# Kernel optimization log

Measured on AMD Instinct MI355X. Metric: run time of the kernel, lower is better.

## Reference

```python
import jax, jax.numpy as jnp
import numpy as np

N, E = 50000, 800000
IN_C, EDGE_IN, HID, HEADS = 16, 16, 32, 4


def setup_inputs() -> dict:
    key = jax.random.key(0)
    ks = jax.random.split(key, 16)
    HC = HEADS * HID
    def lin(k, fan_in, shape):
        b = 1.0 / np.sqrt(fan_in)
        return jax.random.uniform(k, shape, jnp.float32, -b, b)
    return {
        "x": jax.random.normal(ks[0], (N, IN_C), jnp.float32),
        "edge_index": jax.random.randint(ks[1], (2, E), 0, N, jnp.int64),
        "edge_attr": jax.random.normal(ks[2], (E, EDGE_IN), jnp.float32),
        # TransformerConv params
        "Wq": lin(ks[3], IN_C, (IN_C, HC)), "bq": lin(ks[4], IN_C, (HC,)),
        "Wk": lin(ks[5], IN_C, (IN_C, HC)), "bk": lin(ks[6], IN_C, (HC,)),
        "Wv": lin(ks[7], IN_C, (IN_C, HC)), "bv": lin(ks[8], IN_C, (HC,)),
        "We": lin(ks[9], EDGE_IN, (EDGE_IN, HC)),  # lin_edge has no bias in PyG
        "Wskip": lin(ks[10], IN_C, (IN_C, HID)), "bskip": lin(ks[11], IN_C, (HID,)),
        # edge MLP params
        "W1": lin(ks[12], 2 * HID + EDGE_IN, (2 * HID + EDGE_IN, HID)),
        "b1": lin(ks[13], 2 * HID + EDGE_IN, (HID,)),
        "W2": lin(ks[14], HID, (HID, 1)), "b2": lin(ks[15], HID, (1,)),
    }


def _forward(x, edge_attr, Wq, bq, Wk, bk, Wv, bv, We, Wskip, bskip, W1, b1, W2, b2, src, dst):
    n = x.shape[0]
    q = (x @ Wq + bq).reshape(n, HEADS, HID)
    k = (x @ Wk + bk).reshape(n, HEADS, HID)
    v = (x @ Wv + bv).reshape(n, HEADS, HID)
    e = (edge_attr @ We).reshape(-1, HEADS, HID)  # [E,H,C]
    kj = k[src] + e                               # key of source node + edge emb
    alpha = jnp.einsum('ehc,ehc->eh', q[dst], kj) / jnp.sqrt(jnp.float32(HID))
    # segment softmax over incoming edges of each dst node (per head)
    m = jax.ops.segment_max(alpha, dst, num_segments=n)      # [N,H]
    a = jnp.exp(alpha - m[dst])
    s = jax.ops.segment_sum(a, dst, num_segments=n)          # [N,H]
    a = a / s[dst]
    msg = (v[src] + e) * a[:, :, None]                        # [E,H,C]
    out = jax.ops.segment_sum(msg, dst, num_segments=n)      # [N,H,C]
    out = out.mean(axis=1)                                    # concat=False -> mean over heads
    out = out + x @ Wskip + bskip                              # root/skip connection
    # edge MLP on gather-concat features
    feat = jnp.concatenate([out[src], edge_attr, out[dst]], axis=-1)
    h = jax.nn.relu(feat @ W1 + b1)
    return (h @ W2 + b2).reshape(-1)


def reference(x, edge_index, edge_attr, Wq, bq, Wk, bk, Wv, bv, We, Wskip, bskip, W1, b1, W2, b2):
    src, dst = edge_index[0], edge_index[1]
    return _forward(x, edge_attr, Wq, bq, Wk, bk, Wv, bv, We, Wskip, bskip, W1, b1, W2, b2, src, dst)
```

## Files before the change

### kernel.cpp

```cpp
#include <hip/hip_runtime.h>
#include <hip/hip_fp16.h>

#define NN 50000
#define NE 800000
#define NB 196
#define EPB 3125
#define NODE_BLOCKS 12500

#define SL 0.25506413f

#define PMV 0
#define MEV 1024
#define BEV 2048
#define UPV 2112
#define WPV 2176
#define WCV 2240
#define P_TOTAL 2304

template <int CTRL>
__device__ __forceinline__ float dpp_add(float v) {
  int m = __builtin_amdgcn_update_dpp(0, __builtin_bit_cast(int, v), CTRL, 0xF, 0xF, true);
  return v + __builtin_bit_cast(float, m);
}
__device__ __forceinline__ float row16_reduce(float v) {
  v = dpp_add<0xB1>(v);
  v = dpp_add<0x4E>(v);
  v = dpp_add<0x124>(v);
  v = dpp_add<0x128>(v);
  return v;
}

__global__ __launch_bounds__(256) void precompute_kernel(
    const float* __restrict__ Wq, const float* __restrict__ Wk,
    const float* __restrict__ bq, const float* __restrict__ bk,
    const float* __restrict__ We, float* __restrict__ P) {
  int t = threadIdx.x;
  for (int idx = t; idx < 1024; idx += 256) {
    int lane = idx >> 4, i = idx & 15;
    int h = lane >> 4, tt = lane & 15;
    float am = 0.f, ae = 0.f;
#pragma unroll
    for (int c = 0; c < 32; c++) {
      float wq = Wq[i * 128 + h * 32 + c];
      am += wq * Wk[tt * 128 + h * 32 + c];
      ae += wq * We[tt * 128 + h * 32 + c];
    }
    P[PMV + idx] = am * SL;
    P[MEV + idx] = ae * SL;
  }
  if (t < 64) {
    int h = t >> 4, tt = t & 15;
    float be = 0.f, up = 0.f, wp = 0.f;
#pragma unroll
    for (int c = 0; c < 32; c++) {
      be += bq[h * 32 + c] * We[tt * 128 + h * 32 + c];
      up += Wq[tt * 128 + h * 32 + c] * bk[h * 32 + c];
      wp += bq[h * 32 + c] * Wk[tt * 128 + h * 32 + c];
    }
    P[BEV + t] = be * SL;
    P[UPV + t] = up * SL;
    P[WPV + t] = wp * SL;
  }
  if (t < 4) {
    float wc = 0.f;
#pragma unroll
    for (int c = 0; c < 32; c++) wc += bq[t * 32 + c] * bk[t * 32 + c];
    P[WCV + t] = wc * SL;
  }
}

__global__ __launch_bounds__(256) void node_linear_kernel(
    const float* __restrict__ x, const float* __restrict__ P,
    const int* __restrict__ ei, int* __restrict__ hist_all,
    float* __restrict__ y, float* __restrict__ qe,
    float* __restrict__ u4, float* __restrict__ w4) {
  __shared__ int hist[NB];
  if (blockIdx.x >= NODE_BLOCKS) {
    int b = blockIdx.x - NODE_BLOCKS;
    int t = threadIdx.x;
    if (t < NB) hist[t] = 0;
    __syncthreads();
    int base = b * EPB;
    for (int i = t; i < EPB; i += 256)
      atomicAdd(&hist[ei[NE + base + i] >> 8], 1);
    __syncthreads();
    if (t < NB) hist_all[t * 256 + b] = hist[t];
    return;
  }
  int wave = threadIdx.x >> 6;
  int lane = threadIdx.x & 63;
  int n = blockIdx.x * 4 + wave;
  int h = lane >> 4, t = lane & 15;

  const float4* xp = (const float4*)(x + n * 16);
  float4 X0 = xp[0], X1 = xp[1], X2 = xp[2], X3 = xp[3];
  float xr[16] = {X0.x, X0.y, X0.z, X0.w, X1.x, X1.y, X1.z, X1.w,
                  X2.x, X2.y, X2.z, X2.w, X3.x, X3.y, X3.z, X3.w};

  const float4* pm = (const float4*)(P + PMV) + lane * 4;
  const float4* me = (const float4*)(P + MEV) + lane * 4;
  float yt = 0.f, qv = P[BEV + lane];
#pragma unroll
  for (int i4 = 0; i4 < 4; i4++) {
    float4 m = pm[i4], e = me[i4];
    yt += xr[4 * i4] * m.x + xr[4 * i4 + 1] * m.y
        + xr[4 * i4 + 2] * m.z + xr[4 * i4 + 3] * m.w;
    qv += xr[4 * i4] * e.x + xr[4 * i4 + 1] * e.y
        + xr[4 * i4 + 2] * e.z + xr[4 * i4 + 3] * e.w;
  }
  y[n * 64 + lane] = yt;
  qe[n * 64 + lane] = qv;

  float pu = P[UPV + lane] * xr[t];
  float pw = P[WPV + lane] * xr[t];
  pu = row16_reduce(pu);
  pw = row16_reduce(pw);
  if (t == 0) {
    u4[n * 4 + h] = pu;
    w4[n * 4 + h] = pw + P[WCV + h];
  }
}

__global__ __launch_bounds__(256) void scan_buckets_kernel(
    int* __restrict__ hist_all, int* __restrict__ btot) {
  int wv = blockIdx.x * 4 + (threadIdx.x >> 6);
  int l = threadIdx.x & 63;
  if (wv >= NB) return;
  int base = wv * 256;
  int run = 0;
#pragma unroll
  for (int c = 0; c < 4; c++) {
    int v = hist_all[base + c * 64 + l];
    int orig = v;
#pragma unroll
    for (int d = 1; d < 64; d <<= 1) {
      int u = __shfl_up(v, d);
      if (l >= d) v += u;
    }
    hist_all[base + c * 64 + l] = run + v - orig;
    run += __shfl(v, 63);
  }
  if (l == 0) btot[wv] = run;
}

__global__ __launch_bounds__(256) void tiny_scan_kernel(
    const int* __restrict__ btot, int* __restrict__ coarse_offs) {
  __shared__ int sc[256];
  int t = threadIdx.x;
  int v = (t < NB) ? btot[t] : 0;
  sc[t] = v;
  __syncthreads();
  for (int d = 1; d < 256; d <<= 1) {
    int u = (t >= d) ? sc[t - d] : 0;
    __syncthreads();
    sc[t] += u;
    __syncthreads();
  }
  if (t < NB) coarse_offs[t] = sc[t] - v;
  if (t == NB - 1) coarse_offs[NB] = sc[t];
}

__global__ __launch_bounds__(256) void bucket_scatter_kernel(
    const int* __restrict__ ei, const int* __restrict__ cursor_all,
    const int* __restrict__ coarse_offs, int2* __restrict__ s_tmp) {
  __shared__ int cur[NB];
  int t = threadIdx.x, b = blockIdx.x;
  if (t < NB) cur[t] = cursor_all[t * 256 + b] + coarse_offs[t];
  __syncthreads();
  int base = b * EPB;
  for (int i = t; i < EPB; i += 256) {
    int e = base + i;
    int src = ei[e], dst = ei[NE + e];
    int pos = atomicAdd(&cur[dst >> 8], 1);
    s_tmp[pos] = make_int2(src | ((dst & 255) << 16), e);
  }
}

__global__ __launch_bounds__(256) void fine_csr_kernel(
    const int2* __restrict__ s_tmp, const int* __restrict__ coarse_offs,
    int2* __restrict__ s_se, int* __restrict__ csrpos,
    int* __restrict__ offs) {
  __shared__ int cnt[256], sc[256], cur[256];
  int t = threadIdx.x, b = blockIdx.x;
  int lo = coarse_offs[b], hi = coarse_offs[b + 1];
  cnt[t] = 0;
  __syncthreads();
  for (int p = lo + t; p < hi; p += 256)
    atomicAdd(&cnt[(s_tmp[p].x >> 16) & 255], 1);
  __syncthreads();
  int myc = cnt[t];
  sc[t] = myc;
  __syncthreads();
  for (int d = 1; d < 256; d <<= 1) {
    int v = (t >= d) ? sc[t - d] : 0;
    __syncthreads();
    sc[t] += v;
    __syncthreads();
  }
  int excl = sc[t] - myc;
  cur[t] = lo + excl;
  int gd = b * 256 + t;
  if (gd <= NN) offs[gd] = lo + excl;
  __syncthreads();
  for (int p = lo + t; p < hi; p += 256) {
    int2 m = s_tmp[p];
    int pos = atomicAdd(&cur[(m.x >> 16) & 255], 1);
    s_se[pos] = make_int2(m.x & 0xFFFF, m.y);
    csrpos[m.y] = pos;
  }
}

__global__ __launch_bounds__(256) void ea_place_kernel(
    const float* __restrict__ edge_attr, const int* __restrict__ csrpos,
    uint4* __restrict__ s_ea4) {
  int e = blockIdx.x * 256 + threadIdx.x;
  const float4* eap = (const float4*)(edge_attr + (size_t)e * 16);
  float4 a = eap[0], bb = eap[1], c = eap[2], d = eap[3];
  uint4 u0, u1;
  __half2 hh;
  hh = __floats2half2_rn(a.x, a.y);   u0.x = *(unsigned*)&hh;
  hh = __floats2half2_rn(a.z, a.w);   u0.y = *(unsigned*)&hh;
  hh = __floats2half2_rn(bb.x, bb.y); u0.z = *(unsigned*)&hh;
  hh = __floats2half2_rn(bb.z, bb.w); u0.w = *(unsigned*)&hh;
  hh = __floats2half2_rn(c.x, c.y);   u1.x = *(unsigned*)&hh;
  hh = __floats2half2_rn(c.z, c.w);   u1.y = *(unsigned*)&hh;
  hh = __floats2half2_rn(d.x, d.y);   u1.z = *(unsigned*)&hh;
  hh = __floats2half2_rn(d.z, d.w);   u1.w = *(unsigned*)&hh;
  int pos = csrpos[e];
  s_ea4[(size_t)pos * 2]     = u0;
  s_ea4[(size_t)pos * 2 + 1] = u1;
}

__global__ __launch_bounds__(256) void aggregate_kernel(
    const float* __restrict__ y, const float* __restrict__ qe,
    const float* __restrict__ u4, const float* __restrict__ w4,
    const float* __restrict__ x, const __half* __restrict__ s_ea,
    const int2* __restrict__ s_se,
    const float* __restrict__ We, const float* __restrict__ Wv,
    const float* __restrict__ bv,
    const float* __restrict__ Wskip, const float* __restrict__ bskip,
    const float* __restrict__ W1, const float* __restrict__ b1,
    const int* __restrict__ offs,
    __half* __restrict__ Ah, __half* __restrict__ Cbh) {
  int wave = threadIdx.x >> 6, lane = threadIdx.x & 63;
  int n = blockIdx.x * 4 + wave;
  int h = lane >> 4, t = lane & 15;
  int base = h * 32 + t;
  int gb = lane & 48;

  float yt = y[n * 64 + lane];
  float qet = qe[n * 64 + lane];
  float u_n = u4[n * 4 + h];
  int off = offs[n], end = offs[n + 1];

  float s = 0.f, ax = 0.f, ae = 0.f;
  int j = off;
  for (; j + 8 <= end; j += 8) {
    const uint4* sp = (const uint4*)&s_se[j];
    uint4 sa = sp[0], sb = sp[1], sc4 = sp[2], sd = sp[3];
    int src[8] = {(int)sa.x, (int)sa.z, (int)sb.x, (int)sb.z,
                  (int)sc4.x, (int)sc4.z, (int)sd.x, (int)sd.z};
    float xs[8], ea[8], uw[8];
#pragma unroll
    for (int u = 0; u < 8; u++) {
      xs[u] = x[(unsigned)src[u] * 16u + (unsigned)t];
      ea[u] = __half2float(s_ea[(size_t)(j + u) * 16 + t]);
      uw[u] = w4[(unsigned)src[u] * 4u + (unsigned)h];
    }
    float p[8];
#pragma unroll
    for (int u = 0; u < 8; u++) p[u] = fmaf(yt, xs[u], qet * ea[u]);
#pragma unroll
    for (int u = 0; u < 8; u++) p[u] = row16_reduce(p[u]);
#pragma unroll
    for (int u = 0; u < 8; u++) {
      float wgt = exp2f(p[u] + u_n + uw[u]);
      s += wgt;
      ax = fmaf(wgt, xs[u], ax);
      ae = fmaf(wgt, ea[u], ae);
    }
  }
  for (; j < end; j++) {
    int srcu = s_se[j].x;
    float xs = x[(unsigned)srcu * 16u + (unsigned)t];
    float ea_ = __half2float(s_ea[(size_t)j * 16 + t]);
    float uw = w4[(unsigned)srcu * 4u + (unsigned)h];
    float p = fmaf(yt, xs, qet * ea_);
    p = row16_reduce(p);
    float wgt = exp2f(p + u_n + uw);
    s += wgt;
    ax = fmaf(wgt, xs, ax);
    ae = fmaf(wgt, ea_, ae);
  }

  float inv = (end > off) ? 1.f / s : 0.f;
  float dflag = (end > off) ? 1.f : 0.f;
  float axn = ax * inv, aen = ae * inv;
  float r0 = dflag * bv[base], r1 = dflag * bv[base + 16];
#pragma unroll
  for (int i = 0; i < 16; i++) {
    float axi = __shfl(axn, gb | i);
    float aei = __shfl(aen, gb | i);
    r0 += axi * Wv[i * 128 + base]      + aei * We[i * 128 + base];
    r1 += axi * Wv[i * 128 + base + 16] + aei * We[i * 128 + base + 16];
  }
  r0 += __shfl_xor(r0, 16); r0 += __shfl_xor(r0, 32);
  r1 += __shfl_xor(r1, 16); r1 += __shfl_xor(r1, 32);

  float sk0 = bskip[t], sk1 = bskip[t + 16];
#pragma unroll
  for (int i = 0; i < 16; i++) {
    float xi = x[n * 16 + i];
    sk0 += xi * Wskip[i * 32 + t];
    sk1 += xi * Wskip[i * 32 + t + 16];
  }
  float o0 = 0.25f * r0 + sk0;
  float o1 = 0.25f * r1 + sk1;

  int jj = lane & 31;
  int roff = (lane < 32) ? 0 : 48;
  float acc = (lane < 32) ? 0.f : b1[jj];
#pragma unroll
  for (int i = 0; i < 16; i++) {
    float oi = __shfl(o0, i);
    acc += oi * W1[(roff + i) * 32 + jj];
  }
#pragma unroll
  for (int i = 0; i < 16; i++) {
    float oi = __shfl(o1, i);
    acc += oi * W1[(roff + 16 + i) * 32 + jj];
  }
  float nb = __shfl_xor(acc, 1);
  if ((lane & 1) == 0) {
    __half2 hh = __floats2half2_rn(acc, nb);
    if (lane < 32) *(__half2*)(Ah  + n * 32 + jj) = hh;
    else           *(__half2*)(Cbh + n * 32 + jj) = hh;
  }
}

__global__ __launch_bounds__(256) void mlp_kernel(
    const int2* __restrict__ s_se, const __half* __restrict__ s_ea,
    const int* __restrict__ offs,
    const __half* __restrict__ Ah, const __half* __restrict__ Cbh,
    const float* __restrict__ W1, const float* __restrict__ W2,
    const float* __restrict__ b2v, float* __restrict__ out) {
  int wave = threadIdx.x >> 6, lane = threadIdx.x & 63;
  int n = blockIdx.x * 4 + wave;
  int g = lane >> 5, l = lane & 31;

  float w1e[16];
#pragma unroll
  for (int i = 0; i < 16; i++) w1e[i] = W1[(32 + i) * 32 + l];
  float w2j = W2[l];
  float b2s = b2v[0];
  float cb = __half2float(Cbh[n * 32 + l]);
  int off = offs[n], end = offs[n + 1];

  for (int p = off + g; p < end; p += 2) {
    int2 se = s_se[p];
    float a = __half2float(Ah[(unsigned)se.x * 32u + l]);
    const uint4* eap = (const uint4*)(s_ea + (size_t)p * 16);
    uint4 u0 = eap[0], u1 = eap[1];
    float hsum = a + cb;
    const __half2* hp0 = (const __half2*)&u0;
    const __half2* hp1 = (const __half2*)&u1;
#pragma unroll
    for (int i = 0; i < 4; i++) {
      float2 f0 = __half22float2(hp0[i]);
      hsum += f0.x * w1e[2 * i] + f0.y * w1e[2 * i + 1];
      float2 f1 = __half22float2(hp1[i]);
      hsum += f1.x * w1e[8 + 2 * i] + f1.y * w1e[8 + 2 * i + 1];
    }
    float hv = fmaxf(hsum, 0.f) * w2j;
    hv = row16_reduce(hv);
    hv += __shfl_xor(hv, 16);
    if (l == 0) out[se.y] = hv + b2s;
  }
}

extern "C" void kernel_launch(void* const* d_in, const int* in_sizes, int n_in,
                              void* d_out, int out_size, void* d_ws, size_t ws_size,
                              hipStream_t stream) {
  const float* x         = (const float*)d_in[0];
  const int*   ei        = (const int*)d_in[1];
  const float* edge_attr = (const float*)d_in[2];
  const float* Wq = (const float*)d_in[3],  *bq = (const float*)d_in[4];
  const float* Wk = (const float*)d_in[5],  *bk = (const float*)d_in[6];
  const float* Wv = (const float*)d_in[7],  *bv = (const float*)d_in[8];
  const float* We = (const float*)d_in[9];
  const float* Wskip = (const float*)d_in[10], *bskip = (const float*)d_in[11];
  const float* W1 = (const float*)d_in[12], *b1 = (const float*)d_in[13];
  const float* W2 = (const float*)d_in[14], *b2 = (const float*)d_in[15];
  float* out = (float*)d_out;

  char* w = (char*)d_ws;
  float*   y    = (float*)w;            w += (size_t)NN * 64 * 4;
  float*   qe   = (float*)w;            w += (size_t)NN * 64 * 4;
  float*   u4   = (float*)w;            w += (size_t)NN * 4 * 4;
  float*   w4   = (float*)w;            w += (size_t)NN * 4 * 4;
  int2*    s_se = (int2*)w;             w += (size_t)NE * 8;
  int2*    s_tmp = (int2*)w;
  __half*  Ah   = (__half*)s_tmp;
  __half*  Cbh  = (__half*)((char*)s_tmp + (size_t)NN * 32 * 2);
  w += (size_t)NE * 8;
  uint4*   s_ea4 = (uint4*)w;           w += (size_t)NE * 32;
  int*     csrpos = (int*)w;            w += (size_t)NE * 4;
  int*     hist_all = (int*)w;          w += (size_t)256 * 256 * 4;
  int*     btot = (int*)w;              w += 256 * 4;
  int*     coarse_offs = (int*)w;       w += 256 * 4;
  int*     offs = (int*)w;              w += ((size_t)NN + 1) * 4;
  float*   P    = (float*)w;            w += (size_t)P_TOTAL * 4;

  precompute_kernel<<<1, 256, 0, stream>>>(Wq, Wk, bq, bk, We, P);
  node_linear_kernel<<<NODE_BLOCKS + 256, 256, 0, stream>>>(
      x, P, ei, hist_all, y, qe, u4, w4);
  scan_buckets_kernel<<<49, 256, 0, stream>>>(hist_all, btot);
  tiny_scan_kernel<<<1, 256, 0, stream>>>(btot, coarse_offs);
  bucket_scatter_kernel<<<256, 256, 0, stream>>>(ei, hist_all, coarse_offs,
                                                 s_tmp);
  fine_csr_kernel<<<NB, 256, 0, stream>>>(s_tmp, coarse_offs, s_se, csrpos,
                                          offs);
  ea_place_kernel<<<NE / 256, 256, 0, stream>>>(edge_attr, csrpos, s_ea4);
  aggregate_kernel<<<NN / 4, 256, 0, stream>>>(y, qe, u4, w4, x,
                                               (const __half*)s_ea4, s_se,
                                               We, Wv, bv, Wskip, bskip, W1, b1,
                                               offs, Ah, Cbh);
  mlp_kernel<<<NN / 4, 256, 0, stream>>>(s_se, (const __half*)s_ea4, offs,
                                         Ah, Cbh, W1, W2, b2, out);
}
```

Before: 253.9 us.

## Fold per-source bias term into destination query vector and unroll MLP edge loop

The per-source-node scalar w4 (bq·Wk x_src plus a constant) is rewritten algebraically: its x-dependent part is added to the destination-side vector y, so the dot product with x_src already includes it, and the constant joins the per-destination offset. This removes the w4 buffer, its computation in the node kernel, and one random gather per edge in the aggregation loop. Separately, the MLP edge loop now processes two edges per half-wave per iteration to expose more memory-level parallelism. The algebra is exact up to float rounding, and the unrolling adds register pressure.

```diff
diff --git a/kernel.cpp b/kernel.cpp
--- a/kernel.cpp
+++ b/kernel.cpp
@@ -73,7 +73,7 @@
     const float* __restrict__ x, const float* __restrict__ P,
     const int* __restrict__ ei, int* __restrict__ hist_all,
     float* __restrict__ y, float* __restrict__ qe,
-    float* __restrict__ u4, float* __restrict__ w4) {
+    float* __restrict__ u4) {
   __shared__ int hist[NB];
   if (blockIdx.x >= NODE_BLOCKS) {
     int b = blockIdx.x - NODE_BLOCKS;
@@ -112,13 +112,8 @@
   qe[n * 64 + lane] = qv;
 
   float pu = P[UPV + lane] * xr[t];
-  float pw = P[WPV + lane] * xr[t];
   pu = row16_reduce(pu);
-  pw = row16_reduce(pw);
-  if (t == 0) {
-    u4[n * 4 + h] = pu;
-    w4[n * 4 + h] = pw + P[WCV + h];
-  }
+  if (t == 0) u4[n * 4 + h] = pu;
 }
 
 __global__ __launch_bounds__(256) void scan_buckets_kernel(
@@ -233,9 +228,9 @@
 
 __global__ __launch_bounds__(256) void aggregate_kernel(
     const float* __restrict__ y, const float* __restrict__ qe,
-    const float* __restrict__ u4, const float* __restrict__ w4,
+    const float* __restrict__ u4,
     const float* __restrict__ x, const __half* __restrict__ s_ea,
-    const int2* __restrict__ s_se,
+    const int2* __restrict__ s_se, const float* __restrict__ P,
     const float* __restrict__ We, const float* __restrict__ Wv,
     const float* __restrict__ bv,
     const float* __restrict__ Wskip, const float* __restrict__ bskip,
@@ -248,9 +243,9 @@
   int base = h * 32 + t;
   int gb = lane & 48;
 
-  float yt = y[n * 64 + lane];
+  float yt2 = y[n * 64 + lane] + P[WPV + lane];
   float qet = qe[n * 64 + lane];
-  float u_n = u4[n * 4 + h];
+  float un_wc = u4[n * 4 + h] + P[WCV + h];
   int off = offs[n], end = offs[n + 1];
 
   float s = 0.f, ax = 0.f, ae = 0.f;
@@ -260,21 +255,20 @@
     uint4 sa = sp[0], sb = sp[1], sc4 = sp[2], sd = sp[3];
     int src[8] = {(int)sa.x, (int)sa.z, (int)sb.x, (int)sb.z,
                   (int)sc4.x, (int)sc4.z, (int)sd.x, (int)sd.z};
-    float xs[8], ea[8], uw[8];
+    float xs[8], ea[8];
 #pragma unroll
     for (int u = 0; u < 8; u++) {
       xs[u] = x[(unsigned)src[u] * 16u + (unsigned)t];
       ea[u] = __half2float(s_ea[(size_t)(j + u) * 16 + t]);
-      uw[u] = w4[(unsigned)src[u] * 4u + (unsigned)h];
     }
     float p[8];
 #pragma unroll
-    for (int u = 0; u < 8; u++) p[u] = fmaf(yt, xs[u], qet * ea[u]);
+    for (int u = 0; u < 8; u++) p[u] = fmaf(yt2, xs[u], qet * ea[u]);
 #pragma unroll
     for (int u = 0; u < 8; u++) p[u] = row16_reduce(p[u]);
 #pragma unroll
     for (int u = 0; u < 8; u++) {
-      float wgt = exp2f(p[u] + u_n + uw[u]);
+      float wgt = exp2f(p[u] + un_wc);
       s += wgt;
       ax = fmaf(wgt, xs[u], ax);
       ae = fmaf(wgt, ea[u], ae);
@@ -284,10 +278,9 @@
     int srcu = s_se[j].x;
     float xs = x[(unsigned)srcu * 16u + (unsigned)t];
     float ea_ = __half2float(s_ea[(size_t)j * 16 + t]);
-    float uw = w4[(unsigned)srcu * 4u + (unsigned)h];
-    float p = fmaf(yt, xs, qet * ea_);
+    float p = fmaf(yt2, xs, qet * ea_);
     p = row16_reduce(p);
-    float wgt = exp2f(p + u_n + uw);
+    float wgt = exp2f(p + un_wc);
     s += wgt;
     ax = fmaf(wgt, xs, ax);
     ae = fmaf(wgt, ea_, ae);
@@ -356,7 +349,39 @@
   float cb = __half2float(Cbh[n * 32 + l]);
   int off = offs[n], end = offs[n + 1];
 
-  for (int p = off + g; p < end; p += 2) {
+  int p = off + g;
+  for (; p + 2 < end; p += 4) {
+    int2 se0 = s_se[p];
+    int2 se1 = s_se[p + 2];
+    float a0 = __half2float(Ah[(unsigned)se0.x * 32u + l]);
+    float a1 = __half2float(Ah[(unsigned)se1.x * 32u + l]);
+    const uint4* e0p = (const uint4*)(s_ea + (size_t)p * 16);
+    const uint4* e1p = (const uint4*)(s_ea + (size_t)(p + 2) * 16);
+    uint4 u00 = e0p[0], u01 = e0p[1];
+    uint4 u10 = e1p[0], u11 = e1p[1];
+    float h0 = a0 + cb, h1 = a1 + cb;
+    const __half2* q00 = (const __half2*)&u00;
+    const __half2* q01 = (const __half2*)&u01;
+    const __half2* q10 = (const __half2*)&u10;
+    const __half2* q11 = (const __half2*)&u11;
+#pragma unroll
+    for (int i = 0; i < 4; i++) {
+      float2 f;
+      f = __half22float2(q00[i]); h0 += f.x * w1e[2*i]   + f.y * w1e[2*i+1];
+      f = __half22float2(q01[i]); h0 += f.x * w1e[8+2*i] + f.y * w1e[8+2*i+1];
+      f = __half22float2(q10[i]); h1 += f.x * w1e[2*i]   + f.y * w1e[2*i+1];
+      f = __half22float2(q11[i]); h1 += f.x * w1e[8+2*i] + f.y * w1e[8+2*i+1];
+    }
+    float v0 = fmaxf(h0, 0.f) * w2j;
+    float v1 = fmaxf(h1, 0.f) * w2j;
+    v0 = row16_reduce(v0); v1 = row16_reduce(v1);
+    v0 += __shfl_xor(v0, 16); v1 += __shfl_xor(v1, 16);
+    if (l == 0) {
+      out[se0.y] = v0 + b2s;
+      out[se1.y] = v1 + b2s;
+    }
+  }
+  if (p < end) {
     int2 se = s_se[p];
     float a = __half2float(Ah[(unsigned)se.x * 32u + l]);
     const uint4* eap = (const uint4*)(s_ea + (size_t)p * 16);
@@ -397,7 +422,6 @@
   float*   y    = (float*)w;            w += (size_t)NN * 64 * 4;
   float*   qe   = (float*)w;            w += (size_t)NN * 64 * 4;
   float*   u4   = (float*)w;            w += (size_t)NN * 4 * 4;
-  float*   w4   = (float*)w;            w += (size_t)NN * 4 * 4;
   int2*    s_se = (int2*)w;             w += (size_t)NE * 8;
   int2*    s_tmp = (int2*)w;
   __half*  Ah   = (__half*)s_tmp;
@@ -413,7 +437,7 @@
 
   precompute_kernel<<<1, 256, 0, stream>>>(Wq, Wk, bq, bk, We, P);
   node_linear_kernel<<<NODE_BLOCKS + 256, 256, 0, stream>>>(
-      x, P, ei, hist_all, y, qe, u4, w4);
+      x, P, ei, hist_all, y, qe, u4);
   scan_buckets_kernel<<<49, 256, 0, stream>>>(hist_all, btot);
   tiny_scan_kernel<<<1, 256, 0, stream>>>(btot, coarse_offs);
   bucket_scatter_kernel<<<256, 256, 0, stream>>>(ei, hist_all, coarse_offs,
@@ -421,8 +445,8 @@
   fine_csr_kernel<<<NB, 256, 0, stream>>>(s_tmp, coarse_offs, s_se, csrpos,
                                           offs);
   ea_place_kernel<<<NE / 256, 256, 0, stream>>>(edge_attr, csrpos, s_ea4);
-  aggregate_kernel<<<NN / 4, 256, 0, stream>>>(y, qe, u4, w4, x,
-                                               (const __half*)s_ea4, s_se,
+  aggregate_kernel<<<NN / 4, 256, 0, stream>>>(y, qe, u4, x,
+                                               (const __half*)s_ea4, s_se, P,
                                                We, Wv, bv, Wskip, bskip, W1, b1,
                                                offs, Ah, Cbh);
   mlp_kernel<<<NN / 4, 256, 0, stream>>>(s_se, (const __half*)s_ea4, offs,
```

After: 229.3 us. 9.7% less time.
